# Kernel optimization log

Hardware: AMD Instinct MI355X
Metric: run time of the kernel (lower is better)

Reference implementation:

```python
import jax, jax.numpy as jnp
import numpy as np

NUM_HEADS = 16


def setup_inputs() -> dict:
    key = jax.random.key(0)
    ks = jax.random.split(key, 6)
    B, S, E = 2, 2048, 1024
    scale = 1.0 / np.sqrt(E)
    return {
        "x": jax.random.normal(ks[0], (B, S, E), dtype=jnp.float32),
        "mask": jnp.ones((B, S), dtype=jnp.int32),
        "Wq": jax.random.normal(ks[1], (E, E), dtype=jnp.float32) * scale,
        "bq": jnp.zeros((E,), dtype=jnp.float32),
        "Wk": jax.random.normal(ks[2], (E, E), dtype=jnp.float32) * scale,
        "bk": jnp.zeros((E,), dtype=jnp.float32),
        "Wv": jax.random.normal(ks[3], (E, E), dtype=jnp.float32) * scale,
        "bv": jnp.zeros((E,), dtype=jnp.float32),
        "Wo": jax.random.normal(ks[4], (E, E), dtype=jnp.float32) * scale,
        "bo": jnp.zeros((E,), dtype=jnp.float32),
    }


def reference(x, mask, Wq, bq, Wk, bk, Wv, bv, Wo, bo):
    B, S, E = x.shape
    H = NUM_HEADS
    D = E // H

    def heads(t):  # [B,S,E] -> [B,H,S,D]
        return t.reshape(B, S, H, D).transpose(0, 2, 1, 3)

    q = heads(x @ Wq + bq)
    k = heads(x @ Wk + bk)
    v = heads(x @ Wv + bv)

    # scaled dot-product scores [B,H,S,S]
    scores = jnp.einsum("bhsd,bhtd->bhst", q, k) / jnp.sqrt(jnp.float32(D))
    m = mask.astype(jnp.float32)[:, None, None, :]  # key-side padding mask
    scores = scores + (-1e9) * (1.0 - m)
    weights = jax.nn.softmax(scores, axis=-1)
    attn = jnp.einsum("bhst,bhtd->bhsd", weights, v)

    concat = attn.transpose(0, 2, 1, 3).reshape(B, S, E)
    return concat @ Wo + bo
```

## Files before the change

### kernel.cpp

```cpp
#include <hip/hip_runtime.h>
#include <stdint.h>

#define E_DIM   1024
#define HNUM    16
#define DH      64
#define BATCH   2
#define SEQ     2048
#define M_TOT   (BATCH*SEQ)
#define LOG2E   1.44269504088896340736f

typedef __bf16 bf16x8 __attribute__((ext_vector_type(8)));
typedef __bf16 bf16x4 __attribute__((ext_vector_type(4)));
typedef float  f32x4  __attribute__((ext_vector_type(4)));
typedef float  f32x16 __attribute__((ext_vector_type(16)));
typedef unsigned short u16;
typedef unsigned int   u32;
typedef unsigned long long u64;
typedef u16 u16x8 __attribute__((ext_vector_type(8)));
typedef u32 u32x2 __attribute__((ext_vector_type(2)));

__device__ __forceinline__ u16 f2bf(float f) {
    u32 u = __builtin_bit_cast(u32, f);
    u32 r = 0x7FFFu + ((u >> 16) & 1u);
    return (u16)((u + r) >> 16);
}

__device__ __forceinline__ void gload_lds16(const u16* g, u16* l) {
    __builtin_amdgcn_global_load_lds(
        (const __attribute__((address_space(1))) u32*)g,
        (__attribute__((address_space(3))) u32*)l, 16, 0, 0);
}

#define MFMA16(a,b,c) __builtin_amdgcn_mfma_f32_16x16x32_bf16((a),(b),(c),0,0,0)
#define MFMA32(a,b,c) __builtin_amdgcn_mfma_f32_32x32x16_bf16((a),(b),(c),0,0,0)

__global__ __launch_bounds__(256) void cast_x_kernel(const float* __restrict__ x,
                                                     u16* __restrict__ out, int n) {
    int idx = (blockIdx.x * 256 + threadIdx.x) * 4;
    if (idx < n) {
        float4 v = *reinterpret_cast<const float4*>(x + idx);
        ushort4 o;
        o.x = f2bf(v.x); o.y = f2bf(v.y); o.z = f2bf(v.z); o.w = f2bf(v.w);
        *reinterpret_cast<ushort4*>(out + idx) = o;
    }
}

__global__ __launch_bounds__(256) void maskbits_kernel(const int* __restrict__ mask,
                                                       u64* __restrict__ bits) {
    int i = blockIdx.x * 256 + threadIdx.x;
    u64 bl = __ballot(mask[i] != 0);
    if ((i & 63) == 0) bits[i >> 6] = bl;
}

__global__ void wtrans_kernel(const float* __restrict__ w0, const float* __restrict__ w1,
                              const float* __restrict__ w2, const float* __restrict__ w3,
                              u16* __restrict__ out) {
    __shared__ float tile[32][33];
    const float* w = blockIdx.z == 0 ? w0 : blockIdx.z == 1 ? w1 : blockIdx.z == 2 ? w2 : w3;
    const int n0 = blockIdx.x * 32, k0 = blockIdx.y * 32;
    #pragma unroll
    for (int j = 0; j < 4; j++) {
        int k = k0 + threadIdx.y + j * 8;
        tile[threadIdx.y + j * 8][threadIdx.x] = w[(size_t)k * E_DIM + n0 + threadIdx.x];
    }
    __syncthreads();
    u16* o = out + (size_t)blockIdx.z * E_DIM * E_DIM;
    #pragma unroll
    for (int j = 0; j < 4; j++) {
        int n = n0 + threadIdx.y + j * 8;
        o[(size_t)n * E_DIM + k0 + threadIdx.x] = f2bf(tile[threadIdx.x][threadIdx.y + j * 8]);
    }
}

template <typename OutT>
__global__ __launch_bounds__(256) void gemm_kernel(
    const u16* __restrict__ A, const u16* __restrict__ Bt_base, OutT* __restrict__ C_base,
    const float* __restrict__ bias0, const float* __restrict__ bias1,
    const float* __restrict__ bias2, float scale0, int Mdim) {
    const int z = blockIdx.z;
    const u16* Bt = Bt_base + (size_t)z * E_DIM * E_DIM;
    OutT* C = C_base + (size_t)z * Mdim * E_DIM;
    const float* bias = (z == 0) ? bias0 : (z == 1 ? bias1 : bias2);
    const float scale = (z == 0) ? scale0 : 1.0f;

    __shared__ __align__(16) u16 Als[128 * 32];
    __shared__ __align__(16) u16 Bls[128 * 32];

    const int tid = threadIdx.x;
    const int lane = tid & 63;
    const int w = tid >> 6;
    const int wr = (w >> 1) * 64, wc = (w & 1) * 64;
    const int tm = blockIdx.y * 128, tn = blockIdx.x * 128;
    const int r4 = tid >> 2;
    const int c8 = (tid & 3) * 8;

    f32x4 acc[4][4] = {};

    for (int k0 = 0; k0 < E_DIM; k0 += 32) {
        gload_lds16(A + (size_t)(tm + r4) * E_DIM + k0 + c8, Als + tid * 8);
        gload_lds16(A + (size_t)(tm + 64 + r4) * E_DIM + k0 + c8, Als + 2048 + tid * 8);
        gload_lds16(Bt + (size_t)(tn + r4) * E_DIM + k0 + c8, Bls + tid * 8);
        gload_lds16(Bt + (size_t)(tn + 64 + r4) * E_DIM + k0 + c8, Bls + 2048 + tid * 8);
        __syncthreads();
        const int lr = lane & 15, lg = lane >> 4;
        bf16x8 af[4], bfr[4];
        #pragma unroll
        for (int m = 0; m < 4; m++)
            af[m] = *reinterpret_cast<const bf16x8*>(Als + (wr + m * 16 + lr) * 32 + lg * 8);
        #pragma unroll
        for (int n = 0; n < 4; n++)
            bfr[n] = *reinterpret_cast<const bf16x8*>(Bls + (wc + n * 16 + lr) * 32 + lg * 8);
        #pragma unroll
        for (int m = 0; m < 4; m++)
            #pragma unroll
            for (int n = 0; n < 4; n++)
                acc[m][n] = MFMA16(af[m], bfr[n], acc[m][n]);
        __syncthreads();
    }

    const int lr = lane & 15, lg = lane >> 4;
    #pragma unroll
    for (int m = 0; m < 4; m++) {
        #pragma unroll
        for (int n = 0; n < 4; n++) {
            const int col = tn + wc + n * 16 + lr;
            const float bv = bias[col];
            #pragma unroll
            for (int r = 0; r < 4; r++) {
                const int row = tm + wr + m * 16 + lg * 4 + r;
                float v = (acc[m][n][r] + bv) * scale;
                if constexpr (sizeof(OutT) == 2) {
                    C[(size_t)row * E_DIM + col] = f2bf(v);
                } else {
                    C[(size_t)row * E_DIM + col] = v;
                }
            }
        }
    }
}

__global__ __launch_bounds__(256) void attn_kernel(
    const u16* __restrict__ Q, const u16* __restrict__ K, const u16* __restrict__ V,
    const u64* __restrict__ mbits, u16* __restrict__ Out) {
    __shared__ __align__(16) u16 Kls[2][64 * 64];
    __shared__ __align__(16) u16 Vt[2][64 * 64];

    const int tid = threadIdx.x;
    const int lane = tid & 63;
    const int w = tid >> 6;
    const int hi = lane >> 5;
    const int l31 = lane & 31;
    const int h = blockIdx.x, qt = blockIdx.y, b = blockIdx.z;

    const int qrow = b * SEQ + qt * 128 + w * 32 + l31;
    bf16x8 qf[4];
    #pragma unroll
    for (int kc = 0; kc < 4; kc++)
        qf[kc] = *reinterpret_cast<const bf16x8*>(Q + (size_t)qrow * E_DIM + h * DH + kc * 16 + hi * 8);

    const int krow = (l31 & 3) | ((l31 & 4) << 1) | ((l31 & 8) >> 1) | (l31 & 16);
    const u32 ksw = (u32)(krow & 7) << 4;

    const int krA = tid >> 3;
    const int kcA = (tid & 7) ^ (krA & 7);
    const size_t kgoffA = (size_t)krA * E_DIM + kcA * 8;
    const size_t kgoffB = kgoffA + (size_t)32 * E_DIM;

    const int vc = tid & 7;
    const int vs = ((tid >> 3) ^ (vc << 2)) & 31;
    const size_t vgoff = (size_t)(2 * vs) * E_DIM + vc * 8;

    f32x16 oacc0 = {}, oacc1 = {};
    float l_run = 0.f;

    const u16* Kg = K + (size_t)(b * SEQ) * E_DIM + h * DH;
    const u16* Vg = V + (size_t)(b * SEQ) * E_DIM + h * DH;

    gload_lds16(Kg + kgoffA, &Kls[0][tid * 8]);
    gload_lds16(Kg + kgoffB, &Kls[0][(tid + 256) * 8]);
    {
        u16x8 a0 = __builtin_bit_cast(u16x8, *reinterpret_cast<const bf16x8*>(Vg + vgoff));
        u16x8 a1 = __builtin_bit_cast(u16x8, *reinterpret_cast<const bf16x8*>(Vg + vgoff + E_DIM));
        #pragma unroll
        for (int j = 0; j < 8; j++) {
            const u32 off = (((u32)(vc * 8 + j) * 128) + (u32)vs * 4) ^ ((u32)j << 4);
            *(u32*)((char*)Vt[0] + off) = (u32)a0[j] | ((u32)a1[j] << 16);
        }
    }
    __syncthreads();

    const int NT = SEQ / 64;
    for (int kt = 0; kt < NT; kt++) {
        const int cur = kt & 1, nxt = cur ^ 1;
        u16x8 a0, a1;
        if (kt + 1 < NT) {
            const u16* kg = Kg + (size_t)(kt + 1) * 64 * E_DIM;
            const u16* vg = Vg + (size_t)(kt + 1) * 64 * E_DIM;
            gload_lds16(kg + kgoffA, &Kls[nxt][tid * 8]);
            gload_lds16(kg + kgoffB, &Kls[nxt][(tid + 256) * 8]);
            a0 = __builtin_bit_cast(u16x8, *reinterpret_cast<const bf16x8*>(vg + vgoff));
            a1 = __builtin_bit_cast(u16x8, *reinterpret_cast<const bf16x8*>(vg + vgoff + E_DIM));
        }

        const char* Kb = (const char*)Kls[cur];
        f32x16 s0 = {}, s1 = {};
        #pragma unroll
        for (int kc = 0; kc < 4; kc++) {
            const u32 off = (((u32)krow * 128) + (u32)kc * 32 + (u32)hi * 16) ^ ksw;
            bf16x8 kf0 = *(const bf16x8*)(Kb + off);
            bf16x8 kf1 = *(const bf16x8*)(Kb + off + 4096);
            s0 = MFMA32(kf0, qf[kc], s0);
            s1 = MFMA32(kf1, qf[kc], s1);
        }

        const u64 mb = mbits[b * (SEQ / 64) + kt];
        if (mb != ~0ull) {
            #pragma unroll
            for (int r = 0; r < 16; r++) {
                const int key = (r & 3) + 4 * ((r >> 2) & 1) + 8 * hi + 16 * ((r >> 3) & 1);
                if (!((mb >> key) & 1))        s0[r] += -1.442695e9f;
                if (!((mb >> (32 + key)) & 1)) s1[r] += -1.442695e9f;
            }
        }

        float sum = 0.f;
        #pragma unroll
        for (int r = 0; r < 16; r++) { s0[r] = exp2f(s0[r]); sum += s0[r]; }
        #pragma unroll
        for (int r = 0; r < 16; r++) { s1[r] = exp2f(s1[r]); sum += s1[r]; }
        l_run += sum;

        bf16x8 pf[4];
        #pragma unroll
        for (int kc = 0; kc < 4; kc++) {
            #pragma unroll
            for (int e = 0; e < 8; e++) {
                const float v = (kc < 2) ? s0[(kc & 1) * 8 + e] : s1[(kc & 1) * 8 + e];
                pf[kc][e] = (__bf16)v;
            }
        }

        {
            const char* Vb = (const char*)Vt[cur];
            #pragma unroll
            for (int kc = 0; kc < 4; kc++) {
                const u32 roff = (((u32)l31 * 128) + (u32)(2 * kc + hi) * 16) ^ ((u32)(l31 & 7) << 4);
                bf16x8 vf0 = *(const bf16x8*)(Vb + roff);
                bf16x8 vf1 = *(const bf16x8*)(Vb + roff + 4096);
                oacc0 = MFMA32(vf0, pf[kc], oacc0);
                oacc1 = MFMA32(vf1, pf[kc], oacc1);
            }
        }

        if (kt + 1 < NT) {
            #pragma unroll
            for (int j = 0; j < 8; j++) {
                const u32 off = (((u32)(vc * 8 + j) * 128) + (u32)vs * 4) ^ ((u32)j << 4);
                *(u32*)((char*)Vt[nxt] + off) = (u32)a0[j] | ((u32)a1[j] << 16);
            }
        }
        __syncthreads();
    }

    const float l_tot = l_run + __shfl_xor(l_run, 32);
    const float rl = 1.0f / l_tot;
    u16* op = Out + (size_t)qrow * E_DIM + h * DH;
    #pragma unroll
    for (int db = 0; db < 2; db++) {
        #pragma unroll
        for (int j = 0; j < 4; j++) {
            bf16x4 pk;
            #pragma unroll
            for (int c = 0; c < 4; c++) {
                const float v = (db ? oacc1[4 * j + c] : oacc0[4 * j + c]) * rl;
                pk[c] = (__bf16)v;
            }
            const int d0 = 32 * db + 8 * j + 4 * hi;
            *reinterpret_cast<u32x2*>(op + d0) = __builtin_bit_cast(u32x2, pk);
        }
    }
}

extern "C" void kernel_launch(void* const* d_in, const int* in_sizes, int n_in,
                              void* d_out, int out_size, void* d_ws, size_t ws_size,
                              hipStream_t stream) {
    const float* x  = (const float*)d_in[0];
    const int* mask = (const int*)d_in[1];
    const float* Wq = (const float*)d_in[2];
    const float* bq = (const float*)d_in[3];
    const float* Wk = (const float*)d_in[4];
    const float* bk = (const float*)d_in[5];
    const float* Wv = (const float*)d_in[6];
    const float* bv = (const float*)d_in[7];
    const float* Wo = (const float*)d_in[8];
    const float* bo = (const float*)d_in[9];
    float* out = (float*)d_out;

    u16* ws  = (u16*)d_ws;
    const size_t ME = (size_t)M_TOT * E_DIM;
    u16* xb  = ws;
    u16* wt  = ws + ME;
    u16* qb  = ws + 2 * ME;
    u16* kbf = ws + 3 * ME;
    u16* vbf = ws + 4 * ME;
    u64* mbf = (u64*)(ws + 5 * ME);
    u16* ab  = xb;

    cast_x_kernel<<<dim3(M_TOT * E_DIM / 1024), dim3(256), 0, stream>>>(x, xb, M_TOT * E_DIM);
    wtrans_kernel<<<dim3(E_DIM / 32, E_DIM / 32, 4), dim3(32, 8), 0, stream>>>(Wq, Wk, Wv, Wo, wt);
    maskbits_kernel<<<dim3(M_TOT / 256), dim3(256), 0, stream>>>(mask, mbf);
    gemm_kernel<u16><<<dim3(E_DIM / 128, M_TOT / 128, 3), dim3(256), 0, stream>>>(
        xb, wt, qb, bq, bk, bv, 0.125f * LOG2E, M_TOT);
    attn_kernel<<<dim3(HNUM, SEQ / 128, BATCH), dim3(256), 0, stream>>>(qb, kbf, vbf, mbf, ab);
    gemm_kernel<float><<<dim3(E_DIM / 128, M_TOT / 128, 1), dim3(256), 0, stream>>>(
        ab, wt + (size_t)3 * E_DIM * E_DIM, out, bo, bo, bo, 1.0f, M_TOT);
}
```

Before: 149.7 us.

## Split key tiles across two wave groups per attention block and reduce via LDS

Doubles the attention block to 512 threads, with two 4-wave groups each processing alternating 64-key tiles for the same 128 query rows, using a 4-slot K/V LDS ring. At the end, group 1 writes its partial outputs and row sums to LDS and group 0 combines, normalizes, and stores. The aim is more waves per CU and shorter serial key loops to improve latency hiding. It costs more LDS per block, an extra reduction step, and register pressure from the launch bound.

```diff
diff --git a/kernel.cpp b/kernel.cpp
--- a/kernel.cpp
+++ b/kernel.cpp
@@ -139,20 +139,22 @@
     }
 }
 
-__global__ __launch_bounds__(256) void attn_kernel(
+__global__ __launch_bounds__(512, 4) void attn_kernel(
     const u16* __restrict__ Q, const u16* __restrict__ K, const u16* __restrict__ V,
     const u64* __restrict__ mbits, u16* __restrict__ Out) {
-    __shared__ __align__(16) u16 Kls[2][64 * 64];
-    __shared__ __align__(16) u16 Vt[2][64 * 64];
+    __shared__ __align__(16) u16 Kls[4][64 * 64];
+    __shared__ __align__(16) u16 Vt[4][64 * 64];
 
     const int tid = threadIdx.x;
     const int lane = tid & 63;
     const int w = tid >> 6;
+    const int g = w >> 2;
+    const int wg = w & 3;
     const int hi = lane >> 5;
     const int l31 = lane & 31;
     const int h = blockIdx.x, qt = blockIdx.y, b = blockIdx.z;
 
-    const int qrow = b * SEQ + qt * 128 + w * 32 + l31;
+    const int qrow = b * SEQ + qt * 128 + wg * 32 + l31;
     bf16x8 qf[4];
     #pragma unroll
     for (int kc = 0; kc < 4; kc++)
@@ -161,13 +163,14 @@
     const int krow = (l31 & 3) | ((l31 & 4) << 1) | ((l31 & 8) >> 1) | (l31 & 16);
     const u32 ksw = (u32)(krow & 7) << 4;
 
-    const int krA = tid >> 3;
-    const int kcA = (tid & 7) ^ (krA & 7);
+    const int t8 = tid & 255;
+    const int half = tid >> 8;
+    const int krA = t8 >> 3;
+    const int kcA = (t8 & 7) ^ (krA & 7);
     const size_t kgoffA = (size_t)krA * E_DIM + kcA * 8;
     const size_t kgoffB = kgoffA + (size_t)32 * E_DIM;
-
-    const int vc = tid & 7;
-    const int vs = ((tid >> 3) ^ (vc << 2)) & 31;
+    const int vc = t8 & 7;
+    const int vs = ((t8 >> 3) ^ (vc << 2)) & 31;
     const size_t vgoff = (size_t)(2 * vs) * E_DIM + vc * 8;
 
     f32x16 oacc0 = {}, oacc1 = {};
@@ -176,33 +179,38 @@
     const u16* Kg = K + (size_t)(b * SEQ) * E_DIM + h * DH;
     const u16* Vg = V + (size_t)(b * SEQ) * E_DIM + h * DH;
 
-    gload_lds16(Kg + kgoffA, &Kls[0][tid * 8]);
-    gload_lds16(Kg + kgoffB, &Kls[0][(tid + 256) * 8]);
     {
-        u16x8 a0 = __builtin_bit_cast(u16x8, *reinterpret_cast<const bf16x8*>(Vg + vgoff));
-        u16x8 a1 = __builtin_bit_cast(u16x8, *reinterpret_cast<const bf16x8*>(Vg + vgoff + E_DIM));
+        const u16* kg = Kg + (size_t)half * 64 * E_DIM;
+        const u16* vg = Vg + (size_t)half * 64 * E_DIM;
+        gload_lds16(kg + kgoffA, &Kls[half][t8 * 8]);
+        gload_lds16(kg + kgoffB, &Kls[half][(t8 + 256) * 8]);
+        u16x8 a0 = __builtin_bit_cast(u16x8, *reinterpret_cast<const bf16x8*>(vg + vgoff));
+        u16x8 a1 = __builtin_bit_cast(u16x8, *reinterpret_cast<const bf16x8*>(vg + vgoff + E_DIM));
         #pragma unroll
         for (int j = 0; j < 8; j++) {
             const u32 off = (((u32)(vc * 8 + j) * 128) + (u32)vs * 4) ^ ((u32)j << 4);
-            *(u32*)((char*)Vt[0] + off) = (u32)a0[j] | ((u32)a1[j] << 16);
+            *(u32*)((char*)Vt[half] + off) = (u32)a0[j] | ((u32)a1[j] << 16);
         }
     }
     __syncthreads();
 
     const int NT = SEQ / 64;
-    for (int kt = 0; kt < NT; kt++) {
-        const int cur = kt & 1, nxt = cur ^ 1;
+    for (int t = 0; t < NT / 2; t++) {
+        const int mt = 2 * t + g;
+        const int ms = mt & 3;
+        const int pt = 2 * t + 2 + half;
+        const int ps = pt & 3;
         u16x8 a0, a1;
-        if (kt + 1 < NT) {
-            const u16* kg = Kg + (size_t)(kt + 1) * 64 * E_DIM;
-            const u16* vg = Vg + (size_t)(kt + 1) * 64 * E_DIM;
-            gload_lds16(kg + kgoffA, &Kls[nxt][tid * 8]);
-            gload_lds16(kg + kgoffB, &Kls[nxt][(tid + 256) * 8]);
+        if (pt < NT) {
+            const u16* kg = Kg + (size_t)pt * 64 * E_DIM;
+            const u16* vg = Vg + (size_t)pt * 64 * E_DIM;
+            gload_lds16(kg + kgoffA, &Kls[ps][t8 * 8]);
+            gload_lds16(kg + kgoffB, &Kls[ps][(t8 + 256) * 8]);
             a0 = __builtin_bit_cast(u16x8, *reinterpret_cast<const bf16x8*>(vg + vgoff));
             a1 = __builtin_bit_cast(u16x8, *reinterpret_cast<const bf16x8*>(vg + vgoff + E_DIM));
         }
 
-        const char* Kb = (const char*)Kls[cur];
+        const char* Kb = (const char*)Kls[ms];
         f32x16 s0 = {}, s1 = {};
         #pragma unroll
         for (int kc = 0; kc < 4; kc++) {
@@ -213,7 +221,7 @@
             s1 = MFMA32(kf1, qf[kc], s1);
         }
 
-        const u64 mb = mbits[b * (SEQ / 64) + kt];
+        const u64 mb = mbits[b * (SEQ / 64) + mt];
         if (mb != ~0ull) {
             #pragma unroll
             for (int r = 0; r < 16; r++) {
@@ -241,7 +249,7 @@
         }
 
         {
-            const char* Vb = (const char*)Vt[cur];
+            const char* Vb = (const char*)Vt[ms];
             #pragma unroll
             for (int kc = 0; kc < 4; kc++) {
                 const u32 roff = (((u32)l31 * 128) + (u32)(2 * kc + hi) * 16) ^ ((u32)(l31 & 7) << 4);
@@ -252,31 +260,54 @@
             }
         }
 
-        if (kt + 1 < NT) {
+        if (pt < NT) {
             #pragma unroll
             for (int j = 0; j < 8; j++) {
                 const u32 off = (((u32)(vc * 8 + j) * 128) + (u32)vs * 4) ^ ((u32)j << 4);
-                *(u32*)((char*)Vt[nxt] + off) = (u32)a0[j] | ((u32)a1[j] << 16);
+                *(u32*)((char*)Vt[ps] + off) = (u32)a0[j] | ((u32)a1[j] << 16);
             }
         }
         __syncthreads();
     }
 
-    const float l_tot = l_run + __shfl_xor(l_run, 32);
-    const float rl = 1.0f / l_tot;
-    u16* op = Out + (size_t)qrow * E_DIM + h * DH;
-    #pragma unroll
-    for (int db = 0; db < 2; db++) {
-        #pragma unroll
-        for (int j = 0; j < 4; j++) {
-            bf16x4 pk;
-            #pragma unroll
-            for (int c = 0; c < 4; c++) {
-                const float v = (db ? oacc1[4 * j + c] : oacc0[4 * j + c]) * rl;
-                pk[c] = (__bf16)v;
-            }
-            const int d0 = 32 * db + 8 * j + 4 * hi;
-            *reinterpret_cast<u32x2*>(op + d0) = __builtin_bit_cast(u32x2, pk);
+    const float l_half = l_run + __shfl_xor(l_run, 32);
+    float* Olds = (float*)Kls;
+    float* llds = (float*)Vt;
+    const int orow = wg * 32 + l31;
+    if (g == 1) {
+        #pragma unroll
+        for (int db = 0; db < 2; db++) {
+            #pragma unroll
+            for (int j = 0; j < 4; j++) {
+                f32x4 v;
+                #pragma unroll
+                for (int c = 0; c < 4; c++)
+                    v[c] = (db ? oacc1[4 * j + c] : oacc0[4 * j + c]);
+                *reinterpret_cast<f32x4*>(&Olds[orow * 64 + 32 * db + 8 * j + 4 * hi]) = v;
+            }
+        }
+        if (hi == 0) llds[orow] = l_half;
+    }
+    __syncthreads();
+    if (g == 0) {
+        const float l_tot = l_half + llds[orow];
+        const float rl = 1.0f / l_tot;
+        u16* op = Out + (size_t)qrow * E_DIM + h * DH;
+        #pragma unroll
+        for (int db = 0; db < 2; db++) {
+            #pragma unroll
+            for (int j = 0; j < 4; j++) {
+                const f32x4 add = *reinterpret_cast<const f32x4*>(
+                    &Olds[orow * 64 + 32 * db + 8 * j + 4 * hi]);
+                bf16x4 pk;
+                #pragma unroll
+                for (int c = 0; c < 4; c++) {
+                    const float v = ((db ? oacc1[4 * j + c] : oacc0[4 * j + c]) + add[c]) * rl;
+                    pk[c] = (__bf16)v;
+                }
+                const int d0 = 32 * db + 8 * j + 4 * hi;
+                *reinterpret_cast<u32x2*>(op + d0) = __builtin_bit_cast(u32x2, pk);
+            }
         }
     }
 }
@@ -311,7 +342,7 @@
     maskbits_kernel<<<dim3(M_TOT / 256), dim3(256), 0, stream>>>(mask, mbf);
     gemm_kernel<u16><<<dim3(E_DIM / 128, M_TOT / 128, 3), dim3(256), 0, stream>>>(
         xb, wt, qb, bq, bk, bv, 0.125f * LOG2E, M_TOT);
-    attn_kernel<<<dim3(HNUM, SEQ / 128, BATCH), dim3(256), 0, stream>>>(qb, kbf, vbf, mbf, ab);
+    attn_kernel<<<dim3(HNUM, SEQ / 128, BATCH), dim3(512), 0, stream>>>(qb, kbf, vbf, mbf, ab);
     gemm_kernel<float><<<dim3(E_DIM / 128, M_TOT / 128, 1), dim3(256), 0, stream>>>(
         ab, wt + (size_t)3 * E_DIM * E_DIM, out, bo, bo, bo, 1.0f, M_TOT);
 }
```

Measured after the change: 166.4 us. 1.11x slower.

## Split attention key range in two halves and combine partial outputs

Applied to the files above, without the earlier changes.

The attention kernel now processes half of the key sequence per block, doubling the grid. Each block writes an unnormalized bf16 partial output and its row sum. A new combine kernel adds the two partials and normalizes by the total sum. The aim is more blocks per CU for better latency hiding and load balance. The cost is an extra launch plus about 24 MB of partial-output traffic, staged in the output buffer as scratch.

```diff
diff --git a/kernel.cpp b/kernel.cpp
--- a/kernel.cpp
+++ b/kernel.cpp
@@ -141,7 +141,7 @@
 
 __global__ __launch_bounds__(256) void attn_kernel(
     const u16* __restrict__ Q, const u16* __restrict__ K, const u16* __restrict__ V,
-    const u64* __restrict__ mbits, u16* __restrict__ Out) {
+    const u64* __restrict__ mbits, u16* __restrict__ PO, float* __restrict__ lws) {
     __shared__ __align__(16) u16 Kls[2][64 * 64];
     __shared__ __align__(16) u16 Vt[2][64 * 64];
 
@@ -150,7 +150,8 @@
     const int w = tid >> 6;
     const int hi = lane >> 5;
     const int l31 = lane & 31;
-    const int h = blockIdx.x, qt = blockIdx.y, b = blockIdx.z;
+    const int h = blockIdx.x, qt = blockIdx.y;
+    const int b = blockIdx.z >> 1, half = blockIdx.z & 1;
 
     const int qrow = b * SEQ + qt * 128 + w * 32 + l31;
     bf16x8 qf[4];
@@ -173,8 +174,8 @@
     f32x16 oacc0 = {}, oacc1 = {};
     float l_run = 0.f;
 
-    const u16* Kg = K + (size_t)(b * SEQ) * E_DIM + h * DH;
-    const u16* Vg = V + (size_t)(b * SEQ) * E_DIM + h * DH;
+    const u16* Kg = K + (size_t)(b * SEQ + half * (SEQ / 2)) * E_DIM + h * DH;
+    const u16* Vg = V + (size_t)(b * SEQ + half * (SEQ / 2)) * E_DIM + h * DH;
 
     gload_lds16(Kg + kgoffA, &Kls[0][tid * 8]);
     gload_lds16(Kg + kgoffB, &Kls[0][(tid + 256) * 8]);
@@ -189,7 +190,7 @@
     }
     __syncthreads();
 
-    const int NT = SEQ / 64;
+    const int NT = SEQ / 2 / 64;
     for (int kt = 0; kt < NT; kt++) {
         const int cur = kt & 1, nxt = cur ^ 1;
         u16x8 a0, a1;
@@ -213,7 +214,7 @@
             s1 = MFMA32(kf1, qf[kc], s1);
         }
 
-        const u64 mb = mbits[b * (SEQ / 64) + kt];
+        const u64 mb = mbits[b * (SEQ / 64) + half * NT + kt];
         if (mb != ~0ull) {
             #pragma unroll
             for (int r = 0; r < 16; r++) {
@@ -263,22 +264,38 @@
     }
 
     const float l_tot = l_run + __shfl_xor(l_run, 32);
-    const float rl = 1.0f / l_tot;
-    u16* op = Out + (size_t)qrow * E_DIM + h * DH;
+    u16* op = PO + ((size_t)half * M_TOT + qrow) * E_DIM + h * DH;
     #pragma unroll
     for (int db = 0; db < 2; db++) {
         #pragma unroll
         for (int j = 0; j < 4; j++) {
             bf16x4 pk;
             #pragma unroll
-            for (int c = 0; c < 4; c++) {
-                const float v = (db ? oacc1[4 * j + c] : oacc0[4 * j + c]) * rl;
-                pk[c] = (__bf16)v;
-            }
+            for (int c = 0; c < 4; c++)
+                pk[c] = (__bf16)(db ? oacc1[4 * j + c] : oacc0[4 * j + c]);
             const int d0 = 32 * db + 8 * j + 4 * hi;
             *reinterpret_cast<u32x2*>(op + d0) = __builtin_bit_cast(u32x2, pk);
         }
     }
+    if (hi == 0) lws[((size_t)half * M_TOT + qrow) * HNUM + h] = l_tot;
+}
+
+__global__ __launch_bounds__(256) void combine_kernel(const u16* __restrict__ PO,
+                                                      const float* __restrict__ lws,
+                                                      u16* __restrict__ ab) {
+    const int i = (blockIdx.x * 256 + threadIdx.x) * 8;
+    const int row = i >> 10;
+    const int h = (i & 1023) >> 6;
+    const float l0 = lws[(size_t)row * HNUM + h];
+    const float l1 = lws[((size_t)M_TOT + row) * HNUM + h];
+    const float rl = 1.0f / (l0 + l1);
+    const bf16x8 a = *reinterpret_cast<const bf16x8*>(PO + i);
+    const bf16x8 c = *reinterpret_cast<const bf16x8*>(PO + (size_t)M_TOT * E_DIM + i);
+    u16x8 o;
+    #pragma unroll
+    for (int j = 0; j < 8; j++)
+        o[j] = f2bf(((float)a[j] + (float)c[j]) * rl);
+    *reinterpret_cast<u16x8*>(ab + i) = o;
 }
 
 extern "C" void kernel_launch(void* const* d_in, const int* in_sizes, int n_in,
@@ -304,14 +321,18 @@
     u16* kbf = ws + 3 * ME;
     u16* vbf = ws + 4 * ME;
     u64* mbf = (u64*)(ws + 5 * ME);
+    float* lws = (float*)(ws + 5 * ME + 8192);
     u16* ab  = xb;
+    u16* po  = (u16*)d_out;
 
     cast_x_kernel<<<dim3(M_TOT * E_DIM / 1024), dim3(256), 0, stream>>>(x, xb, M_TOT * E_DIM);
     wtrans_kernel<<<dim3(E_DIM / 32, E_DIM / 32, 4), dim3(32, 8), 0, stream>>>(Wq, Wk, Wv, Wo, wt);
     maskbits_kernel<<<dim3(M_TOT / 256), dim3(256), 0, stream>>>(mask, mbf);
     gemm_kernel<u16><<<dim3(E_DIM / 128, M_TOT / 128, 3), dim3(256), 0, stream>>>(
         xb, wt, qb, bq, bk, bv, 0.125f * LOG2E, M_TOT);
-    attn_kernel<<<dim3(HNUM, SEQ / 128, BATCH), dim3(256), 0, stream>>>(qb, kbf, vbf, mbf, ab);
+    attn_kernel<<<dim3(HNUM, SEQ / 128, BATCH * 2), dim3(256), 0, stream>>>(
+        qb, kbf, vbf, mbf, po, lws);
+    combine_kernel<<<dim3(M_TOT * E_DIM / 2048), dim3(256), 0, stream>>>(po, lws, ab);
     gemm_kernel<float><<<dim3(E_DIM / 128, M_TOT / 128, 1), dim3(256), 0, stream>>>(
         ab, wt + (size_t)3 * E_DIM * E_DIM, out, bo, bo, bo, 1.0f, M_TOT);
 }
```

After: 153.7 us. 1.03x slower.
